# Optimization experiments

Hardware: AMD Instinct MI355X
Metric: run time of the kernel (lower is better)

The kernel has to match this reference:

```python
import jax, jax.numpy as jnp
import numpy as np

N = 50000      # nodes
E = 800000     # edges (avg degree 16)
B = 8          # graphs in batch
H = 128        # hidden (message_passer out_channels)
FF = 64        # fourier_feat_dim -> fourier features have dim 2*FF
REPEATS = 4    # repeats_training
OUT = 4        # output_dim
IN_X = 5
IN_MASK = 3

def _fourier(x, M):
    # https://arxiv.org/pdf/2106.02795.pdf : [cos(xM), sin(xM)] / sqrt(2F)
    p = x @ M
    return jnp.concatenate([jnp.cos(p), jnp.sin(p)], axis=-1) / jnp.sqrt(2.0 * M.shape[1])

def _seg_mean(v, idx, n):
    s = jax.ops.segment_sum(v, idx, num_segments=n)
    c = jax.ops.segment_sum(jnp.ones((v.shape[0],), v.dtype), idx, num_segments=n)
    return s / jnp.maximum(c, 1.0)[:, None]

def setup_inputs() -> dict:
    key = jax.random.key(0)
    ks = jax.random.split(key, 16)
    x = jax.random.normal(ks[0], (N, IN_X), jnp.float32)
    x_mask = jax.random.bernoulli(ks[1], 0.1, (N, IN_MASK)).astype(jnp.float32)
    edge_index = jax.random.randint(ks[2], (2, E), 0, N)
    edge_attr = jax.random.normal(ks[3], (E, 3), jnp.float32)
    pos = jax.random.uniform(ks[4], (N, 2), jnp.float32)
    batch = jnp.sort(jax.random.randint(ks[5], (N,), 0, B))
    sampling_points = jax.random.uniform(ks[6], (2,), jnp.float32)
    fourier_mat = jax.random.normal(ks[7], (2, FF), jnp.float32)  # learnable, init N(0,1)
    W_enc = jax.random.normal(ks[8], (IN_X + IN_MASK, H), jnp.float32) * 0.1
    b_enc = jnp.zeros((H,), jnp.float32)
    W_msg = jax.random.normal(ks[9], (2 * H + 3, H), jnp.float32) * 0.05
    b_msg = jnp.zeros((H,), jnp.float32)
    W_upd = jax.random.normal(ks[10], (4 * H, H), jnp.float32) * 0.05
    b_upd = jnp.zeros((H,), jnp.float32)
    W_dec = jax.random.normal(ks[11], (H, OUT), jnp.float32) * 0.1
    b_dec = jnp.zeros((OUT,), jnp.float32)
    return dict(x=x, x_mask=x_mask, edge_index=edge_index, edge_attr=edge_attr,
                pos=pos, batch=batch, sampling_points=sampling_points,
                fourier_mat=fourier_mat, W_enc=W_enc, b_enc=b_enc,
                W_msg=W_msg, b_msg=b_msg, W_upd=W_upd, b_upd=b_upd,
                W_dec=W_dec, b_dec=b_dec)

def reference(x, x_mask, edge_index, edge_attr, pos, batch, sampling_points,
              fourier_mat, W_enc, b_enc, W_msg, b_msg, W_upd, b_upd, W_dec, b_dec):
    bc = x_mask[:, -1]                                   # 0/1 BC flag
    x_full = jnp.concatenate([x, x_mask], axis=1)        # x = concat([x, x_mask])
    keys_ff = _fourier(pos, fourier_mat)                 # input fourier features [N, 2F]
    h = jax.nn.relu(x_full @ W_enc + b_enc)              # encoder -> [N, H]

    # x_BC: scatter-mean over BC nodes per graph (computed once)
    bc_sum = jax.ops.segment_sum(h * bc[:, None], batch, num_segments=B)
    bc_cnt = jax.ops.segment_sum(bc, batch, num_segments=B)
    x_BC = bc_sum / jnp.maximum(bc_cnt, 1.0)[:, None]    # [B, H]

    x_graph = _seg_mean(h, batch, B)                     # global_mean_pool [B, H]
    src, dst = edge_index[0], edge_index[1]
    deg = jnp.maximum(jax.ops.segment_sum(jnp.ones((E,), h.dtype), dst, num_segments=N), 1.0)

    for _ in range(REPEATS):  # repeated message passing
        m = jax.nn.relu(jnp.concatenate([h[src], h[dst], edge_attr], axis=1) @ W_msg + b_msg)
        agg = jax.ops.segment_sum(m, dst, num_segments=N) / deg[:, None]  # scatter-mean
        upd_in = jnp.concatenate([h, agg, x_graph[batch], x_BC[batch]], axis=1)
        h = h + jax.nn.relu(upd_in @ W_upd + b_upd)
        x_graph = _seg_mean(h, batch, B)                 # re-pool each repeat

    decoded = h @ W_dec + b_dec                          # [N, OUT]

    # kernelized fourier-feature interpolation at the sampling point
    q = _fourier(sampling_points, fourier_mat)           # [2F]
    nq = q / jnp.linalg.norm(q)
    nk = keys_ff / jnp.linalg.norm(keys_ff, axis=1, keepdims=True)
    vals_sum = h.sum(axis=0)                             # [H]
    kwv = nk.T @ h                                       # [2F, H]
    ks_sum = nk.sum(axis=0)                              # [2F]
    enc = (vals_sum + nq @ kwv) / (N + nq @ ks_sum)      # [H]
    U_sampled = enc @ W_dec + b_dec                      # [OUT]
    # pack (U_sampled, decoded) into one array: row 0 = sampled point, rows 1: = nodes
    return jnp.concatenate([U_sampled[None, :], decoded], axis=0)
```

## Files before the change

### kernel.cpp

```cpp
#include <hip/hip_runtime.h>
#include <math.h>

#define Nn 50000
#define Ee 800000
#define Bb 8
#define ROUNDS 4
#define KWVB 512
#define SCB 196
#define AP 40
#define HP 132
#define KS 40
#define NBK 196
#define P1B 391
#define CHUNK 2047

typedef __attribute__((ext_vector_type(8))) short bf16x8;
typedef __attribute__((ext_vector_type(4))) float f32x4;

__device__ inline short f2bf(float f) {
  union { float f; unsigned u; } v; v.f = f;
  unsigned r = v.u + 0x7fff + ((v.u >> 16) & 1);
  return (short)(r >> 16);
}
__device__ inline float bf2f(short s) {
  union { float f; unsigned u; } v; v.u = ((unsigned)(unsigned short)s) << 16;
  return v.f;
}

__global__ __launch_bounds__(256) void encode_seg(
    const float* __restrict__ x, const float* __restrict__ xm,
    const int* __restrict__ batch, const float* __restrict__ W,
    const float* __restrict__ b, float* __restrict__ h,
    float* __restrict__ gsum, float* __restrict__ gcnt,
    float* __restrict__ bcsum, float* __restrict__ bccnt) {
  __shared__ float xs5[128 * 5];
  __shared__ float xm3[128 * 3];
  __shared__ float ls[Bb * 128];
  __shared__ float lb[Bb * 128];
  __shared__ float lc[Bb], lbc[Bb];
  const int t = threadIdx.x;
  const int nBase = blockIdx.x * 128;
  const int j = t & 127, half = t >> 7;
  const int base5 = nBase * 5, base3 = nBase * 3;
  for (int q = t; q < 640; q += 256) xs5[q] = (base5 + q < Nn * 5) ? x[base5 + q] : 0.f;
  for (int q = t; q < 384; q += 256) xm3[q] = (base3 + q < Nn * 3) ? xm[base3 + q] : 0.f;
  for (int q = t; q < Bb * 128; q += 256) { ls[q] = 0.f; lb[q] = 0.f; }
  if (t < Bb) { lc[t] = 0.f; lbc[t] = 0.f; }
  float Wcol[8];
#pragma unroll
  for (int k = 0; k < 8; k++) Wcol[k] = W[k * 128 + j];
  const float bj = b[j];
  __syncthreads();
  int curb = -1;
  float runh = 0.f, runb = 0.f, runc = 0.f, runbc = 0.f;
  for (int kk = 0; kk < 64; kk++) {
    int i = nBase + kk * 2 + half;
    if (i >= Nn) break;
    int li = i - nBase;
    float acc = bj;
#pragma unroll
    for (int k = 0; k < 5; k++) acc = fmaf(xs5[li * 5 + k], Wcol[k], acc);
#pragma unroll
    for (int k = 0; k < 3; k++) acc = fmaf(xm3[li * 3 + k], Wcol[5 + k], acc);
    float v = fmaxf(acc, 0.f);
    h[(size_t)i * 128 + j] = v;
    float bc = xm3[li * 3 + 2];
    int g = batch[i];
    if (g != curb) {
      if (curb >= 0) {
        atomicAdd(&ls[curb * 128 + j], runh);
        atomicAdd(&lb[curb * 128 + j], runb);
        if (j == 0) { atomicAdd(&lc[curb], runc); atomicAdd(&lbc[curb], runbc); }
      }
      curb = g; runh = runb = runc = runbc = 0.f;
    }
    runh += v; runb += v * bc;
    if (j == 0) { runc += 1.f; runbc += bc; }
  }
  if (curb >= 0) {
    atomicAdd(&ls[curb * 128 + j], runh);
    atomicAdd(&lb[curb * 128 + j], runb);
    if (j == 0) { atomicAdd(&lc[curb], runc); atomicAdd(&lbc[curb], runbc); }
  }
  __syncthreads();
  for (int q = t; q < Bb * 128; q += 256) {
    float a = ls[q], c = lb[q];
    if (a != 0.f) atomicAdd(&gsum[q], a);
    if (c != 0.f) atomicAdd(&bcsum[q], c);
  }
  if (t < Bb) { atomicAdd(&gcnt[t], lc[t]); atomicAdd(&bccnt[t], lbc[t]); }
}

__global__ __launch_bounds__(256) void split_w_kernel(
    const float* __restrict__ Wm, const float* __restrict__ Wu,
    short* __restrict__ Wmt_h, short* __restrict__ Wmt_l,
    short* __restrict__ Wut_h, short* __restrict__ Wut_l) {
  int idx = blockIdx.x * 256 + threadIdx.x;
  if (idx < 32768) {
    int k = idx & 127, n = (idx >> 7) & 127, y = idx >> 14;
    float w = Wm[(size_t)(y * 128 + k) * 128 + n];
    short hi = f2bf(w);
    Wmt_h[idx] = hi;
    Wmt_l[idx] = f2bf(w - bf2f(hi));
  } else if (idx < 65536) {
    int j = idx - 32768;
    int k = j & 255, n = j >> 8;
    float w = Wu[(size_t)k * 128 + n];
    short hi = f2bf(w);
    Wut_h[j] = hi;
    Wut_l[j] = f2bf(w - bf2f(hi));
  }
}

__global__ __launch_bounds__(256) void bkt_cnt(const int* __restrict__ ei,
                                               int* __restrict__ bktcnt) {
  __shared__ int hist[NBK];
  int t = threadIdx.x;
  for (int q = t; q < NBK; q += 256) hist[q] = 0;
  __syncthreads();
  int base = blockIdx.x * CHUNK;
  int end = base + CHUNK < Ee ? base + CHUNK : Ee;
  for (int e = base + t; e < end; e += 256) atomicAdd(&hist[ei[Ee + e] >> 8], 1);
  __syncthreads();
  for (int q = t; q < NBK; q += 256)
    if (hist[q]) atomicAdd(&bktcnt[q], hist[q]);
}
__global__ __launch_bounds__(256) void bkt_scan(const int* __restrict__ bktcnt,
                                                int* __restrict__ bktbase,
                                                int* __restrict__ bktcur) {
  __shared__ int s[256];
  int t = threadIdx.x;
  int v = (t < NBK) ? bktcnt[t] : 0;
  s[t] = v;
  __syncthreads();
  for (int off = 1; off < 256; off <<= 1) {
    int x = (t >= off) ? s[t - off] : 0;
    __syncthreads();
    s[t] += x;
    __syncthreads();
  }
  int ex = s[t] - v;
  if (t < NBK) { bktbase[t] = ex; bktcur[t] = ex; }
  if (t == NBK - 1) bktbase[NBK] = ex + v;
}
__global__ __launch_bounds__(256) void bkt_part(
    const int* __restrict__ ei, const float* __restrict__ ea,
    int* __restrict__ bktcur, int2* __restrict__ recA,
    unsigned char* __restrict__ dlo) {
  __shared__ int hist[NBK], lbase[NBK], lcur[NBK];
  int t = threadIdx.x;
  for (int q = t; q < NBK; q += 256) hist[q] = 0;
  __syncthreads();
  int base = blockIdx.x * CHUNK;
  int end = base + CHUNK < Ee ? base + CHUNK : Ee;
  for (int e = base + t; e < end; e += 256) atomicAdd(&hist[ei[Ee + e] >> 8], 1);
  __syncthreads();
  for (int q = t; q < NBK; q += 256) {
    int c = hist[q];
    lbase[q] = c ? atomicAdd(&bktcur[q], c) : 0;
    lcur[q] = 0;
  }
  __syncthreads();
  for (int e = base + t; e < end; e += 256) {
    int d = ei[Ee + e];
    int bk = d >> 8;
    int p = lbase[bk] + atomicAdd(&lcur[bk], 1);
    unsigned r0 = (unsigned)ei[e] |
                  ((unsigned)(unsigned short)f2bf(ea[3 * (size_t)e + 0]) << 16);
    unsigned r1 = (unsigned)(unsigned short)f2bf(ea[3 * (size_t)e + 1]) |
                  ((unsigned)(unsigned short)f2bf(ea[3 * (size_t)e + 2]) << 16);
    recA[p] = make_int2((int)r0, (int)r1);
    dlo[p] = (unsigned char)(d & 255);
  }
}
__global__ __launch_bounds__(256) void dst_cnt(const int* __restrict__ bktbase,
                                               const unsigned char* __restrict__ dlo,
                                               int* __restrict__ cnt) {
  __shared__ int hh[256];
  int t = threadIdx.x;
  hh[t] = 0;
  __syncthreads();
  int b = blockIdx.x;
  int lo = bktbase[b], hi = bktbase[b + 1];
  for (int i = lo + t; i < hi; i += 256) atomicAdd(&hh[dlo[i]], 1);
  __syncthreads();
  int d = b * 256 + t;
  if (d < Nn) cnt[d] = hh[t];
}
__global__ __launch_bounds__(256) void bsum_kernel(const int* __restrict__ cnt,
                                                   int* __restrict__ bsum) {
  __shared__ int wsum[4];
  int t = threadIdx.x;
  int i = blockIdx.x * 256 + t;
  int v = (i < Nn) ? cnt[i] : 0;
#pragma unroll
  for (int off = 32; off > 0; off >>= 1) v += __shfl_down(v, off);
  if ((t & 63) == 0) wsum[t >> 6] = v;
  __syncthreads();
  if (t == 0) bsum[blockIdx.x] = wsum[0] + wsum[1] + wsum[2] + wsum[3];
}
__global__ __launch_bounds__(256) void scan_top_kernel(const int* __restrict__ bsum,
                                                       int* __restrict__ boff) {
  __shared__ int s[256];
  int t = threadIdx.x;
  int v = (t < SCB) ? bsum[t] : 0;
  s[t] = v;
  __syncthreads();
  for (int off = 1; off < 256; off <<= 1) {
    int x = (t >= off) ? s[t - off] : 0;
    __syncthreads();
    s[t] += x;
    __syncthreads();
  }
  boff[t] = s[t] - v;
}
__global__ __launch_bounds__(256) void apply_kernel(
    const int* __restrict__ cnt, const int* __restrict__ boff,
    int* __restrict__ rowptr, float* __restrict__ invdeg) {
  __shared__ int s[256];
  int t = threadIdx.x;
  int i = blockIdx.x * 256 + t;
  int v = (i < Nn) ? cnt[i] : 0;
  s[t] = v;
  __syncthreads();
  for (int off = 1; off < 256; off <<= 1) {
    int x = (t >= off) ? s[t - off] : 0;
    __syncthreads();
    s[t] += x;
    __syncthreads();
  }
  int ex = boff[blockIdx.x] + s[t] - v;
  if (i < Nn) {
    rowptr[i] = ex;
    invdeg[i] = 1.0f / fmaxf((float)v, 1.0f);
    if (i == Nn - 1) rowptr[Nn] = ex + v;
  }
}
__global__ __launch_bounds__(256) void bkt_fin(
    const int* __restrict__ bktbase, const int2* __restrict__ recA,
    const unsigned char* __restrict__ dlo, const int* __restrict__ rowptr,
    int2* __restrict__ rec) {
  __shared__ int cur[256];
  int t = threadIdx.x;
  int b = blockIdx.x;
  int d = b * 256 + t;
  cur[t] = (d < Nn) ? rowptr[d] : 0;
  __syncthreads();
  int lo = bktbase[b], hi = bktbase[b + 1];
  for (int i = lo + t; i < hi; i += 256) {
    int dl = dlo[i];
    int p = atomicAdd(&cur[dl], 1);
    rec[p] = recA[i];
  }
}

__global__ __launch_bounds__(128) void gb_static_kernel(
    const float* __restrict__ bcsum, const float* __restrict__ bccnt,
    const float* __restrict__ Wu, const float* __restrict__ bu,
    float* __restrict__ gbst) {
  __shared__ float xb[128];
  int g = blockIdx.x, t = threadIdx.x;
  xb[t] = bcsum[g * 128 + t] / fmaxf(bccnt[g], 1.f);
  __syncthreads();
  float acc = bu[t];
#pragma unroll 4
  for (int k = 0; k < 128; k++) acc = fmaf(xb[k], Wu[(size_t)(384 + k) * 128 + t], acc);
  gbst[g * 128 + t] = acc;
}

__global__ __launch_bounds__(128) void gb_dyn_kernel(
    const float* __restrict__ gsum, const float* __restrict__ gcnt,
    const float* __restrict__ gbst, const float* __restrict__ Wu,
    float* __restrict__ gb) {
  __shared__ float xg[128];
  int g = blockIdx.x, t = threadIdx.x;
  xg[t] = gsum[g * 128 + t] / fmaxf(gcnt[g], 1.f);
  __syncthreads();
  float acc = gbst[g * 128 + t];
#pragma unroll 4
  for (int k = 0; k < 128; k++) acc = fmaf(xg[k], Wu[(size_t)(256 + k) * 128 + t], acc);
  gb[g * 128 + t] = acc;
}

__global__ __launch_bounds__(256) void proj_mfma(
    const float* __restrict__ h, const short* __restrict__ Wth,
    unsigned char* __restrict__ hs8, unsigned short* __restrict__ hdbf) {
  __shared__ short Ah_s[128 * AP];
  __shared__ short Bh_s[128 * AP];
  const int t = threadIdx.x;
  const int nBase = blockIdx.x * 128;
  const int yoff = blockIdx.y * 16384;
  const int wave = t >> 6, lane = t & 63;
  const int ml = lane & 15, quad = lane >> 4;
  const int ko = quad * 8;

  f32x4 acc[2][8];
#pragma unroll
  for (int nt = 0; nt < 2; nt++)
#pragma unroll
    for (int mt = 0; mt < 8; mt++)
#pragma unroll
      for (int q = 0; q < 4; q++) acc[nt][mt][q] = 0.f;

  const int srow = t >> 1;
  const int kc = (t & 1) * 16;
  const int nd0 = nBase + srow;
  const int nn = nd0 < Nn ? nd0 : Nn - 1;

  for (int c = 0; c < 4; c++) {
    const float* p = &h[(size_t)nn * 128 + c * 32 + kc];
    float4 u0 = *(const float4*)(p + 0);
    float4 u1 = *(const float4*)(p + 4);
    float4 u2 = *(const float4*)(p + 8);
    float4 u3 = *(const float4*)(p + 12);
    const int k0 = c * 32;
    const bf16x8 gb0 = *(const bf16x8*)&Wth[(size_t)yoff + srow * 128 + k0 + kc];
    const bf16x8 gb1 = *(const bf16x8*)&Wth[(size_t)yoff + srow * 128 + k0 + kc + 8];
    float xs[16] = {u0.x,u0.y,u0.z,u0.w, u1.x,u1.y,u1.z,u1.w,
                    u2.x,u2.y,u2.z,u2.w, u3.x,u3.y,u3.z,u3.w};
    bf16x8 vh0, vh1;
#pragma unroll
    for (int j = 0; j < 8; j++) vh0[j] = f2bf(xs[j]);
#pragma unroll
    for (int j = 0; j < 8; j++) vh1[j] = f2bf(xs[8 + j]);
    __syncthreads();
    *(bf16x8*)&Ah_s[srow * AP + kc] = vh0;
    *(bf16x8*)&Ah_s[srow * AP + kc + 8] = vh1;
    *(bf16x8*)&Bh_s[srow * AP + kc] = gb0;
    *(bf16x8*)&Bh_s[srow * AP + kc + 8] = gb1;
    __syncthreads();
#pragma unroll
    for (int mt = 0; mt < 8; mt++) {
      const int ar = (mt * 16 + ml) * AP + ko;
      bf16x8 ah = *(const bf16x8*)&Ah_s[ar];
#pragma unroll
      for (int nt = 0; nt < 2; nt++) {
        const int br = (wave * 32 + nt * 16 + ml) * AP + ko;
        bf16x8 bh = *(const bf16x8*)&Bh_s[br];
        acc[nt][mt] = __builtin_amdgcn_mfma_f32_16x16x32_bf16(ah, bh, acc[nt][mt], 0, 0, 0);
      }
    }
  }
  if (blockIdx.y == 0) {
#pragma unroll
    for (int nt = 0; nt < 2; nt++) {
      const int ch = wave * 32 + nt * 16 + ml;
#pragma unroll
      for (int mt = 0; mt < 8; mt++) {
#pragma unroll
        for (int q = 0; q < 4; q++) {
          int nd = nBase + mt * 16 + quad * 4 + q;
          if (nd < Nn) {
            int pk = __builtin_amdgcn_cvt_pk_fp8_f32(acc[nt][mt][q], acc[nt][mt][q], 0, false);
            hs8[(size_t)nd * 128 + ch] = (unsigned char)(pk & 0xff);
          }
        }
      }
    }
  } else {
#pragma unroll
    for (int nt = 0; nt < 2; nt++) {
      const int ch = wave * 32 + nt * 16 + ml;
#pragma unroll
      for (int mt = 0; mt < 8; mt++) {
#pragma unroll
        for (int q = 0; q < 4; q++) {
          int nd = nBase + mt * 16 + quad * 4 + q;
          if (nd < Nn) hdbf[(size_t)nd * 128 + ch] = (unsigned short)f2bf(acc[nt][mt][q]);
        }
      }
    }
  }
}

__global__ __launch_bounds__(256) void agg_kernel(
    const unsigned char* __restrict__ hs8, const unsigned short* __restrict__ hdbf,
    unsigned short* __restrict__ aggbf, const int2* __restrict__ rec,
    const int* __restrict__ rowptr, const float* __restrict__ invdeg,
    const float* __restrict__ Wm, const float* __restrict__ bm) {
  int t = threadIdx.x;
  int hw = t >> 5, lane = t & 31;
  int v = blockIdx.x * 8 + hw;
  if (v >= Nn) return;
  int c0 = lane * 4;
  const float4 We0 = *(const float4*)&Wm[(size_t)256 * 128 + c0];
  const float4 We1 = *(const float4*)&Wm[(size_t)257 * 128 + c0];
  const float4 We2 = *(const float4*)&Wm[(size_t)258 * 128 + c0];
  const float4 b4  = *(const float4*)&bm[c0];
  const ushort4 hd4 = *(const ushort4*)&hdbf[(size_t)v * 128 + c0];
  const float bx = b4.x + bf2f((short)hd4.x), by = b4.y + bf2f((short)hd4.y),
              bz = b4.z + bf2f((short)hd4.z), bw = b4.w + bf2f((short)hd4.w);
  float ax = 0.f, ay = 0.f, az = 0.f, aw = 0.f;
  float ax2 = 0.f, ay2 = 0.f, az2 = 0.f, aw2 = 0.f;
  const int r0 = rowptr[v], r1 = rowptr[v + 1];
  int e = r0;
  for (; e + 2 <= r1; e += 2) {
    int2 q0 = rec[e], q1 = rec[e + 1];
    int s0 = q0.x & 0xffff, s1 = q1.x & 0xffff;
    unsigned hr0 = *(const unsigned*)&hs8[(size_t)s0 * 128 + c0];
    unsigned hr1 = *(const unsigned*)&hs8[(size_t)s1 * 128 + c0];
    float e00 = bf2f((short)(q0.x >> 16));
    float e01 = bf2f((short)(q0.y & 0xffff));
    float e02 = bf2f((short)(q0.y >> 16));
    float e10 = bf2f((short)(q1.x >> 16));
    float e11 = bf2f((short)(q1.y & 0xffff));
    float e12 = bf2f((short)(q1.y >> 16));
    float h0x = __builtin_amdgcn_cvt_f32_fp8(hr0, 0);
    float h0y = __builtin_amdgcn_cvt_f32_fp8(hr0, 1);
    float h0z = __builtin_amdgcn_cvt_f32_fp8(hr0, 2);
    float h0w = __builtin_amdgcn_cvt_f32_fp8(hr0, 3);
    float h1x = __builtin_amdgcn_cvt_f32_fp8(hr1, 0);
    float h1y = __builtin_amdgcn_cvt_f32_fp8(hr1, 1);
    float h1z = __builtin_amdgcn_cvt_f32_fp8(hr1, 2);
    float h1w = __builtin_amdgcn_cvt_f32_fp8(hr1, 3);
    ax += fmaxf(fmaf(e00, We0.x, fmaf(e01, We1.x, fmaf(e02, We2.x, h0x + bx))), 0.f);
    ay += fmaxf(fmaf(e00, We0.y, fmaf(e01, We1.y, fmaf(e02, We2.y, h0y + by))), 0.f);
    az += fmaxf(fmaf(e00, We0.z, fmaf(e01, We1.z, fmaf(e02, We2.z, h0z + bz))), 0.f);
    aw += fmaxf(fmaf(e00, We0.w, fmaf(e01, We1.w, fmaf(e02, We2.w, h0w + bw))), 0.f);
    ax2 += fmaxf(fmaf(e10, We0.x, fmaf(e11, We1.x, fmaf(e12, We2.x, h1x + bx))), 0.f);
    ay2 += fmaxf(fmaf(e10, We0.y, fmaf(e11, We1.y, fmaf(e12, We2.y, h1y + by))), 0.f);
    az2 += fmaxf(fmaf(e10, We0.z, fmaf(e11, We1.z, fmaf(e12, We2.z, h1z + bz))), 0.f);
    aw2 += fmaxf(fmaf(e10, We0.w, fmaf(e11, We1.w, fmaf(e12, We2.w, h1w + bw))), 0.f);
  }
  if (e < r1) {
    int2 q0 = rec[e];
    int s0 = q0.x & 0xffff;
    unsigned hr0 = *(const unsigned*)&hs8[(size_t)s0 * 128 + c0];
    float e00 = bf2f((short)(q0.x >> 16));
    float e01 = bf2f((short)(q0.y & 0xffff));
    float e02 = bf2f((short)(q0.y >> 16));
    float h0x = __builtin_amdgcn_cvt_f32_fp8(hr0, 0);
    float h0y = __builtin_amdgcn_cvt_f32_fp8(hr0, 1);
    float h0z = __builtin_amdgcn_cvt_f32_fp8(hr0, 2);
    float h0w = __builtin_amdgcn_cvt_f32_fp8(hr0, 3);
    ax += fmaxf(fmaf(e00, We0.x, fmaf(e01, We1.x, fmaf(e02, We2.x, h0x + bx))), 0.f);
    ay += fmaxf(fmaf(e00, We0.y, fmaf(e01, We1.y, fmaf(e02, We2.y, h0y + by))), 0.f);
    az += fmaxf(fmaf(e00, We0.z, fmaf(e01, We1.z, fmaf(e02, We2.z, h0z + bz))), 0.f);
    aw += fmaxf(fmaf(e00, We0.w, fmaf(e01, We1.w, fmaf(e02, We2.w, h0w + bw))), 0.f);
  }
  const float idg = invdeg[v];
  ushort4 o;
  o.x = (unsigned short)f2bf((ax + ax2) * idg);
  o.y = (unsigned short)f2bf((ay + ay2) * idg);
  o.z = (unsigned short)f2bf((az + az2) * idg);
  o.w = (unsigned short)f2bf((aw + aw2) * idg);
  *(ushort4*)&aggbf[(size_t)v * 128 + c0] = o;
}

__global__ __launch_bounds__(256) void updg_mfma(
    float* __restrict__ h, const unsigned short* __restrict__ aggbf,
    const int* __restrict__ batch,
    const short* __restrict__ Wth, const short* __restrict__ Wtl,
    const float* __restrict__ gb, float* __restrict__ gsum_out) {
  __shared__ short Ah_s[128 * AP], Al_s[128 * AP];
  __shared__ short Bh_s[128 * AP], Bl_s[128 * AP];
  __shared__ float gbs[Bb * 128];
  __shared__ float ls[Bb * 128];
  const int t = threadIdx.x;
  const int nBase = blockIdx.x * 128;
  *(float4*)&gbs[t * 4] = *(const float4*)&gb[t * 4];
#pragma unroll
  for (int q = 0; q < 4; q++) ls[t + q * 256] = 0.f;

  const int wave = t >> 6, lane = t & 63;
  const int ml = lane & 15, quad = lane >> 4;
  const int ko = quad * 8;

  f32x4 acc[2][8];
#pragma unroll
  for (int nt = 0; nt < 2; nt++)
#pragma unroll
    for (int mt = 0; mt < 8; mt++)
#pragma unroll
      for (int q = 0; q < 4; q++) acc[nt][mt][q] = 0.f;

  const int srow = t >> 1;
  const int kc = (t & 1) * 16;
  const int nd0 = nBase + srow;
  const int nn = nd0 < Nn ? nd0 : Nn - 1;

  for (int c = 0; c < 8; c++) {
    const int k0 = c * 32;
    bf16x8 vh0, vh1, vl0, vl1;
    if (c < 4) {
      const float* p = &h[(size_t)nn * 128 + c * 32 + kc];
      float4 u0 = *(const float4*)(p + 0);
      float4 u1 = *(const float4*)(p + 4);
      float4 u2 = *(const float4*)(p + 8);
      float4 u3 = *(const float4*)(p + 12);
      float xs[16] = {u0.x,u0.y,u0.z,u0.w, u1.x,u1.y,u1.z,u1.w,
                      u2.x,u2.y,u2.z,u2.w, u3.x,u3.y,u3.z,u3.w};
#pragma unroll
      for (int j = 0; j < 8; j++) {
        short hi = f2bf(xs[j]);
        vh0[j] = hi; vl0[j] = f2bf(xs[j] - bf2f(hi));
      }
#pragma unroll
      for (int j = 0; j < 8; j++) {
        short hi = f2bf(xs[8 + j]);
        vh1[j] = hi; vl1[j] = f2bf(xs[8 + j] - bf2f(hi));
      }
    } else {
      const unsigned short* pa = &aggbf[(size_t)nn * 128 + (c - 4) * 32 + kc];
      vh0 = *(const bf16x8*)(pa);
      vh1 = *(const bf16x8*)(pa + 8);
    }
    const bf16x8 gb0 = *(const bf16x8*)&Wth[(size_t)srow * 256 + k0 + kc];
    const bf16x8 gb1 = *(const bf16x8*)&Wth[(size_t)srow * 256 + k0 + kc + 8];
    const bf16x8 gl0 = *(const bf16x8*)&Wtl[(size_t)srow * 256 + k0 + kc];
    const bf16x8 gl1 = *(const bf16x8*)&Wtl[(size_t)srow * 256 + k0 + kc + 8];
    __syncthreads();
    *(bf16x8*)&Ah_s[srow * AP + kc] = vh0;
    *(bf16x8*)&Ah_s[srow * AP + kc + 8] = vh1;
    if (c < 4) {
      *(bf16x8*)&Al_s[srow * AP + kc] = vl0;
      *(bf16x8*)&Al_s[srow * AP + kc + 8] = vl1;
    }
    *(bf16x8*)&Bh_s[srow * AP + kc] = gb0;
    *(bf16x8*)&Bh_s[srow * AP + kc + 8] = gb1;
    *(bf16x8*)&Bl_s[srow * AP + kc] = gl0;
    *(bf16x8*)&Bl_s[srow * AP + kc + 8] = gl1;
    __syncthreads();
    if (c < 4) {
#pragma unroll
      for (int mt = 0; mt < 8; mt++) {
        const int ar = (mt * 16 + ml) * AP + ko;
        bf16x8 ah = *(const bf16x8*)&Ah_s[ar];
        bf16x8 al = *(const bf16x8*)&Al_s[ar];
#pragma unroll
        for (int nt = 0; nt < 2; nt++) {
          const int br = (wave * 32 + nt * 16 + ml) * AP + ko;
          bf16x8 bh = *(const bf16x8*)&Bh_s[br];
          bf16x8 bl = *(const bf16x8*)&Bl_s[br];
          acc[nt][mt] = __builtin_amdgcn_mfma_f32_16x16x32_bf16(ah, bh, acc[nt][mt], 0, 0, 0);
          acc[nt][mt] = __builtin_amdgcn_mfma_f32_16x16x32_bf16(ah, bl, acc[nt][mt], 0, 0, 0);
          acc[nt][mt] = __builtin_amdgcn_mfma_f32_16x16x32_bf16(al, bh, acc[nt][mt], 0, 0, 0);
        }
      }
    } else {
#pragma unroll
      for (int mt = 0; mt < 8; mt++) {
        const int ar = (mt * 16 + ml) * AP + ko;
        bf16x8 ah = *(const bf16x8*)&Ah_s[ar];
#pragma unroll
        for (int nt = 0; nt < 2; nt++) {
          const int br = (wave * 32 + nt * 16 + ml) * AP + ko;
          bf16x8 bh = *(const bf16x8*)&Bh_s[br];
          bf16x8 bl = *(const bf16x8*)&Bl_s[br];
          acc[nt][mt] = __builtin_amdgcn_mfma_f32_16x16x32_bf16(ah, bh, acc[nt][mt], 0, 0, 0);
          acc[nt][mt] = __builtin_amdgcn_mfma_f32_16x16x32_bf16(ah, bl, acc[nt][mt], 0, 0, 0);
        }
      }
    }
  }
#pragma unroll
  for (int nt = 0; nt < 2; nt++) {
    const int ch = wave * 32 + nt * 16 + ml;
#pragma unroll
    for (int mt = 0; mt < 8; mt++) {
      int rbase = nBase + mt * 16 + quad * 4;
      float runv = 0.f;
      int curb = -1;
#pragma unroll
      for (int q = 0; q < 4; q++) {
        int nd = rbase + q;
        if (nd < Nn) {
          int bi = batch[nd];
          float u = fmaxf(acc[nt][mt][q] + gbs[bi * 128 + ch], 0.f);
          float hn = h[(size_t)nd * 128 + ch] + u;
          h[(size_t)nd * 128 + ch] = hn;
          if (bi != curb) {
            if (curb >= 0) atomicAdd(&ls[curb * 128 + ch], runv);
            curb = bi;
            runv = 0.f;
          }
          runv += hn;
        }
      }
      if (curb >= 0) atomicAdd(&ls[curb * 128 + ch], runv);
    }
  }
  __syncthreads();
#pragma unroll
  for (int q = 0; q < 4; q++) {
    int idx = t + q * 256;
    float v = ls[idx];
    if (v != 0.f) atomicAdd(&gsum_out[idx], v);
  }
}

__global__ __launch_bounds__(256) void kwv_kernel(
    const float* __restrict__ h, const float* __restrict__ pos,
    const float* __restrict__ Fm, const float* __restrict__ Wd,
    const float* __restrict__ bd, float* __restrict__ partial,
    float* __restrict__ ksum, float* __restrict__ out) {
  __shared__ float h_s[32 * HP];
  __shared__ short nkT[128 * KS];
  __shared__ short hT[128 * KS];
  __shared__ float wd[512];
  __shared__ float ksum_s[128];
  __shared__ float dsum[256];
  const int t = threadIdx.x;
  const int hr = t >> 3;
  const int hc = (t & 7) * 16;
  const int fg = (t & 7) * 8;
  const int wave = t >> 6, lane = t & 63;
  const int ml = lane & 15, quad = lane >> 4;
  const int ko = quad * 8;
  if (t < 128) { *(float4*)&wd[t * 4] = *(const float4*)&Wd[t * 4]; ksum_s[t] = 0.f; }
  const float bdv = bd[t & 3];
  const int dn = (t & 127) >> 2, dno = t & 3;
  const int dk0 = (t >> 7) * 64;
  f32x4 acc[2][8];
#pragma unroll
  for (int nt = 0; nt < 2; nt++)
#pragma unroll
    for (int mt = 0; mt < 8; mt++)
#pragma unroll
      for (int q = 0; q < 4; q++) acc[nt][mt][q] = 0.f;
  float klc[8], kls[8];
#pragma unroll
  for (int f = 0; f < 8; f++) { klc[f] = 0.f; kls[f] = 0.f; }

  int ptile = -1;
  const int nTiles = (Nn + 31) / 32;
  for (int tile = blockIdx.x; tile < nTiles; tile += gridDim.x) {
    const int gh = tile * 32 + hr;
    float4 hv0 = {0.f, 0.f, 0.f, 0.f}, hv1 = hv0, hv2 = hv0, hv3 = hv0;
    float cbuf[8], sbuf[8];
    if (gh < Nn) {
      const float* hp = &h[(size_t)gh * 128 + hc];
      hv0 = *(const float4*)(hp + 0);
      hv1 = *(const float4*)(hp + 4);
      hv2 = *(const float4*)(hp + 8);
      hv3 = *(const float4*)(hp + 12);
      const float px = pos[gh * 2 + 0], py = pos[gh * 2 + 1];
#pragma unroll
      for (int f = 0; f < 8; f++) {
        float p = px * Fm[fg + f] + py * Fm[64 + fg + f];
        cbuf[f] = cosf(p) * 0.125f;
        sbuf[f] = sinf(p) * 0.125f;
      }
    } else {
#pragma unroll
      for (int f = 0; f < 8; f++) { cbuf[f] = 0.f; sbuf[f] = 0.f; }
    }
    float xs[16] = {hv0.x,hv0.y,hv0.z,hv0.w, hv1.x,hv1.y,hv1.z,hv1.w,
                    hv2.x,hv2.y,hv2.z,hv2.w, hv3.x,hv3.y,hv3.z,hv3.w};
    __syncthreads();
    if (ptile >= 0 && t < 128) {
      int gn = ptile * 32 + dn;
      if (gn < Nn) out[4 + (size_t)gn * 4 + dno] = dsum[t] + dsum[t + 128] + bdv;
    }
    *(float4*)&h_s[hr * HP + hc + 0]  = hv0;
    *(float4*)&h_s[hr * HP + hc + 4]  = hv1;
    *(float4*)&h_s[hr * HP + hc + 8]  = hv2;
    *(float4*)&h_s[hr * HP + hc + 12] = hv3;
#pragma unroll
    for (int i = 0; i < 16; i++) hT[(hc + i) * KS + hr] = f2bf(xs[i]);
#pragma unroll
    for (int f = 0; f < 8; f++) {
      nkT[(fg + f) * KS + hr] = f2bf(cbuf[f]);
      nkT[(64 + fg + f) * KS + hr] = f2bf(sbuf[f]);
      klc[f] += cbuf[f];
      kls[f] += sbuf[f];
    }
    __syncthreads();
#pragma unroll
    for (int mt = 0; mt < 8; mt++) {
      bf16x8 ah = *(const bf16x8*)&nkT[(mt * 16 + ml) * KS + ko];
#pragma unroll
      for (int nt = 0; nt < 2; nt++) {
        bf16x8 bh = *(const bf16x8*)&hT[(wave * 32 + nt * 16 + ml) * KS + ko];
        acc[nt][mt] = __builtin_amdgcn_mfma_f32_16x16x32_bf16(ah, bh, acc[nt][mt], 0, 0, 0);
      }
    }
    {
      float s = 0.f;
#pragma unroll 4
      for (int kk = dk0; kk < dk0 + 64; kk++) {
        int k = (kk + dn) & 127;
        s = fmaf(h_s[dn * HP + k], wd[k * 4 + dno], s);
      }
      dsum[t] = s;
    }
    ptile = tile;
  }
  __syncthreads();
  if (ptile >= 0 && t < 128) {
    int gn = ptile * 32 + dn;
    if (gn < Nn) out[4 + (size_t)gn * 4 + dno] = dsum[t] + dsum[t + 128] + bdv;
  }
  float* pb = &partial[(size_t)blockIdx.x * 16384];
#pragma unroll
  for (int nt = 0; nt < 2; nt++) {
    const int col = wave * 32 + nt * 16 + ml;
#pragma unroll
    for (int mt = 0; mt < 8; mt++) {
#pragma unroll
      for (int q = 0; q < 4; q++) {
        int row = mt * 16 + quad * 4 + q;
        pb[row * 128 + col] = acc[nt][mt][q];
      }
    }
  }
#pragma unroll
  for (int f = 0; f < 8; f++) {
    atomicAdd(&ksum_s[fg + f], klc[f]);
    atomicAdd(&ksum_s[64 + fg + f], kls[f]);
  }
  __syncthreads();
  if (t < 128) atomicAdd(&ksum[t], ksum_s[t]);
}

__global__ __launch_bounds__(256) void kwv_reduce(const float* __restrict__ partial,
                                                  float* __restrict__ kwv) {
  int idx = blockIdx.x * 256 + threadIdx.x;
  float s = 0.f;
  for (int b = 0; b < KWVB; b++) s += partial[(size_t)b * 16384 + idx];
  kwv[idx] = s;
}

__global__ __launch_bounds__(128) void final_kernel(
    const float* __restrict__ sp, const float* __restrict__ Fm,
    const float* __restrict__ kwv, const float* __restrict__ vs,
    const float* __restrict__ ksum, const float* __restrict__ Wd,
    const float* __restrict__ bd, float* __restrict__ out) {
  __shared__ float nq_s[128];
  __shared__ float red[2];
  __shared__ float redU[8];
  int t = threadIdx.x;
  int jj = t & 63;
  float p = sp[0] * Fm[jj] + sp[1] * Fm[64 + jj];
  nq_s[t] = ((t < 64) ? cosf(p) : sinf(p)) * 0.125f;
  __syncthreads();
  float num = 0.f;
#pragma unroll
  for (int g = 0; g < Bb; g++) num += vs[g * 128 + t];
  for (int k = 0; k < 128; k++) num = fmaf(nq_s[k], kwv[k * 128 + t], num);
  float dp = nq_s[t] * ksum[t];
#pragma unroll
  for (int off = 32; off > 0; off >>= 1) dp += __shfl_down(dp, off);
  if ((t & 63) == 0) red[t >> 6] = dp;
  __syncthreads();
  float den = (float)Nn + red[0] + red[1];
  float e = num / den;
  float u[4];
#pragma unroll
  for (int o = 0; o < 4; o++) u[o] = e * Wd[t * 4 + o];
#pragma unroll
  for (int off = 32; off > 0; off >>= 1) {
#pragma unroll
    for (int o = 0; o < 4; o++) u[o] += __shfl_down(u[o], off);
  }
  if ((t & 63) == 0) {
#pragma unroll
    for (int o = 0; o < 4; o++) redU[(t >> 6) * 4 + o] = u[o];
  }
  __syncthreads();
  if (t < 4) out[t] = redU[t] + redU[4 + t] + bd[t];
}

extern "C" void kernel_launch(void* const* d_in, const int* in_sizes, int n_in,
                              void* d_out, int out_size, void* d_ws, size_t ws_size,
                              hipStream_t stream) {
  const float* x    = (const float*)d_in[0];
  const float* xm   = (const float*)d_in[1];
  const int*   ei   = (const int*)d_in[2];
  const float* ea   = (const float*)d_in[3];
  const float* pos  = (const float*)d_in[4];
  const int*   batch= (const int*)d_in[5];
  const float* sp   = (const float*)d_in[6];
  const float* Fm   = (const float*)d_in[7];
  const float* Wenc = (const float*)d_in[8];
  const float* benc = (const float*)d_in[9];
  const float* Wmsg = (const float*)d_in[10];
  const float* bmsg = (const float*)d_in[11];
  const float* Wupd = (const float*)d_in[12];
  const float* bupd = (const float*)d_in[13];
  const float* Wdec = (const float*)d_in[14];
  const float* bdec = (const float*)d_in[15];
  float* out = (float*)d_out;

  float* ws     = (float*)d_ws;
  float* h      = ws;
  float* agg    = h + (size_t)Nn * 128;
  float* aux    = agg + (size_t)Nn * 128;
  float* invdeg = aux + (size_t)Nn * 128;
  float* gsum   = invdeg + Nn;
  float* gcnt   = gsum + 1024;
  float* bcsum  = gcnt + 8;
  float* bccnt  = bcsum + 1024;
  float* gsumR  = bccnt + 8;
  float* vsum   = gsumR + 4096;
  float* ksum   = vsum + 128;
  float* gbst   = ksum + 128;
  float* gbuf   = gbst + 1024;
  float* kwv    = gbuf + 4096;
  int2*  rec    = (int2*)(kwv + 16384);
  int*   cnt    = (int*)(rec + Ee);
  int*   rowptr = cnt + Nn;
  int*   bsum   = rowptr + Nn + 1;
  int*   boff   = bsum + 256;
  int*   bktcnt = boff + 256;
  int*   bktbase= bktcnt + 196;
  int*   bktcur = bktbase + 197;
  short* wmt_h  = (short*)(bktcur + 196);
  short* wmt_l  = wmt_h + 32768;
  short* wut_h  = wmt_l + 32768;
  short* wut_l  = wut_h + 32768;
  int2*  recA   = (int2*)(wut_l + 32768);
  unsigned char* dlo = (unsigned char*)(recA + Ee);

  unsigned short* aggbf = (unsigned short*)agg;
  unsigned char*  hs8   = (unsigned char*)aux;
  unsigned short* hdbf  = (unsigned short*)(hs8 + (size_t)Nn * 128);

  hipMemsetAsync(gsum, 0, 6416 * sizeof(float), stream);
  hipMemsetAsync(bktcnt, 0, 196 * sizeof(int), stream);

  split_w_kernel<<<256, 256, 0, stream>>>(Wmsg, Wupd, wmt_h, wmt_l, wut_h, wut_l);

  bkt_cnt<<<P1B, 256, 0, stream>>>(ei, bktcnt);
  bkt_scan<<<1, 256, 0, stream>>>(bktcnt, bktbase, bktcur);
  bkt_part<<<P1B, 256, 0, stream>>>(ei, ea, bktcur, recA, dlo);
  dst_cnt<<<NBK, 256, 0, stream>>>(bktbase, dlo, cnt);
  bsum_kernel<<<SCB, 256, 0, stream>>>(cnt, bsum);
  scan_top_kernel<<<1, 256, 0, stream>>>(bsum, boff);
  apply_kernel<<<SCB, 256, 0, stream>>>(cnt, boff, rowptr, invdeg);
  bkt_fin<<<NBK, 256, 0, stream>>>(bktbase, recA, dlo, rowptr, rec);

  const int nb128 = (Nn + 127) / 128;
  encode_seg<<<nb128, 256, 0, stream>>>(x, xm, batch, Wenc, benc, h,
                                        gsum, gcnt, bcsum, bccnt);
  gb_static_kernel<<<Bb, 128, 0, stream>>>(bcsum, bccnt, Wupd, bupd, gbst);
  gb_dyn_kernel<<<Bb, 128, 0, stream>>>(gsum, gcnt, gbst, Wupd, gbuf);

  for (int r = 0; r < ROUNDS; r++) {
    proj_mfma<<<dim3(nb128, 2), 256, 0, stream>>>(h, wmt_h, hs8, hdbf);
    agg_kernel<<<(Nn + 7) / 8, 256, 0, stream>>>(hs8, hdbf, aggbf, rec, rowptr,
                                                 invdeg, Wmsg, bmsg);
    updg_mfma<<<nb128, 256, 0, stream>>>(h, aggbf, batch, wut_h, wut_l,
                                         gbuf + r * 1024, gsumR + r * 1024);
    if (r < ROUNDS - 1)
      gb_dyn_kernel<<<Bb, 128, 0, stream>>>(gsumR + r * 1024, gcnt, gbst, Wupd,
                                            gbuf + (r + 1) * 1024);
  }

  kwv_kernel<<<KWVB, 256, 0, stream>>>(h, pos, Fm, Wdec, bdec, agg, ksum, out);
  kwv_reduce<<<64, 256, 0, stream>>>(agg, kwv);
  final_kernel<<<1, 128, 0, stream>>>(sp, Fm, kwv, gsumR + 3 * 1024, ksum,
                                      Wdec, bdec, out);
}
```

Baseline: 675.5 us.

## Halve MFMA node tile to 64 rows and fuse CSR-build kernels

The projection and update MFMA kernels now process 64 nodes per block instead of 128. This halves the accumulator registers and A-tile shared memory, doubles the grid size for better occupancy across CUs, and re-maps the A-tile loading to four threads per row. Separately, the per-destination count kernel now also emits block sums, and the rowptr apply step is fused with the bucket finalize scatter, removing two launches and a rowptr reload. The trade-off is that each block loads the weight tile once per 64 rows, so weight traffic from L2 doubles.

```diff
diff --git a/kernel.cpp b/kernel.cpp
--- a/kernel.cpp
+++ b/kernel.cpp
@@ -173,10 +173,11 @@
     dlo[p] = (unsigned char)(d & 255);
   }
 }
-__global__ __launch_bounds__(256) void dst_cnt(const int* __restrict__ bktbase,
-                                               const unsigned char* __restrict__ dlo,
-                                               int* __restrict__ cnt) {
+__global__ __launch_bounds__(256) void dst_cnt_bsum(
+    const int* __restrict__ bktbase, const unsigned char* __restrict__ dlo,
+    int* __restrict__ cnt, int* __restrict__ bsum) {
   __shared__ int hh[256];
+  __shared__ int wsum[4];
   int t = threadIdx.x;
   hh[t] = 0;
   __syncthreads();
@@ -185,19 +186,13 @@
   for (int i = lo + t; i < hi; i += 256) atomicAdd(&hh[dlo[i]], 1);
   __syncthreads();
   int d = b * 256 + t;
-  if (d < Nn) cnt[d] = hh[t];
-}
-__global__ __launch_bounds__(256) void bsum_kernel(const int* __restrict__ cnt,
-                                                   int* __restrict__ bsum) {
-  __shared__ int wsum[4];
-  int t = threadIdx.x;
-  int i = blockIdx.x * 256 + t;
-  int v = (i < Nn) ? cnt[i] : 0;
+  int v = hh[t];
+  if (d < Nn) cnt[d] = v;
 #pragma unroll
   for (int off = 32; off > 0; off >>= 1) v += __shfl_down(v, off);
   if ((t & 63) == 0) wsum[t >> 6] = v;
   __syncthreads();
-  if (t == 0) bsum[blockIdx.x] = wsum[0] + wsum[1] + wsum[2] + wsum[3];
+  if (t == 0) bsum[b] = wsum[0] + wsum[1] + wsum[2] + wsum[3];
 }
 __global__ __launch_bounds__(256) void scan_top_kernel(const int* __restrict__ bsum,
                                                        int* __restrict__ boff) {
@@ -214,12 +209,16 @@
   }
   boff[t] = s[t] - v;
 }
-__global__ __launch_bounds__(256) void apply_kernel(
+__global__ __launch_bounds__(256) void apply_fin(
     const int* __restrict__ cnt, const int* __restrict__ boff,
-    int* __restrict__ rowptr, float* __restrict__ invdeg) {
+    const int* __restrict__ bktbase, const int2* __restrict__ recA,
+    const unsigned char* __restrict__ dlo,
+    int* __restrict__ rowptr, float* __restrict__ invdeg,
+    int2* __restrict__ rec) {
   __shared__ int s[256];
-  int t = threadIdx.x;
-  int i = blockIdx.x * 256 + t;
+  __shared__ int cur[256];
+  int t = threadIdx.x, b = blockIdx.x;
+  int i = b * 256 + t;
   int v = (i < Nn) ? cnt[i] : 0;
   s[t] = v;
   __syncthreads();
@@ -229,28 +228,19 @@
     s[t] += x;
     __syncthreads();
   }
-  int ex = boff[blockIdx.x] + s[t] - v;
+  int ex = boff[b] + s[t] - v;
   if (i < Nn) {
     rowptr[i] = ex;
     invdeg[i] = 1.0f / fmaxf((float)v, 1.0f);
     if (i == Nn - 1) rowptr[Nn] = ex + v;
   }
-}
-__global__ __launch_bounds__(256) void bkt_fin(
-    const int* __restrict__ bktbase, const int2* __restrict__ recA,
-    const unsigned char* __restrict__ dlo, const int* __restrict__ rowptr,
-    int2* __restrict__ rec) {
-  __shared__ int cur[256];
-  int t = threadIdx.x;
-  int b = blockIdx.x;
-  int d = b * 256 + t;
-  cur[t] = (d < Nn) ? rowptr[d] : 0;
+  cur[t] = ex;
   __syncthreads();
   int lo = bktbase[b], hi = bktbase[b + 1];
-  for (int i = lo + t; i < hi; i += 256) {
-    int dl = dlo[i];
+  for (int ii = lo + t; ii < hi; ii += 256) {
+    int dl = dlo[ii];
     int p = atomicAdd(&cur[dl], 1);
-    rec[p] = recA[i];
+    rec[p] = recA[ii];
   }
 }
 
@@ -285,52 +275,48 @@
 __global__ __launch_bounds__(256) void proj_mfma(
     const float* __restrict__ h, const short* __restrict__ Wth,
     unsigned char* __restrict__ hs8, unsigned short* __restrict__ hdbf) {
-  __shared__ short Ah_s[128 * AP];
+  __shared__ short Ah_s[64 * AP];
   __shared__ short Bh_s[128 * AP];
   const int t = threadIdx.x;
-  const int nBase = blockIdx.x * 128;
+  const int nBase = blockIdx.x * 64;
   const int yoff = blockIdx.y * 16384;
   const int wave = t >> 6, lane = t & 63;
   const int ml = lane & 15, quad = lane >> 4;
   const int ko = quad * 8;
 
-  f32x4 acc[2][8];
+  f32x4 acc[2][4];
 #pragma unroll
   for (int nt = 0; nt < 2; nt++)
 #pragma unroll
-    for (int mt = 0; mt < 8; mt++)
+    for (int mt = 0; mt < 4; mt++)
 #pragma unroll
       for (int q = 0; q < 4; q++) acc[nt][mt][q] = 0.f;
 
-  const int srow = t >> 1;
+  const int arow = t >> 2;
+  const int kq = (t & 3) * 8;
+  const int brow = t >> 1;
   const int kc = (t & 1) * 16;
-  const int nd0 = nBase + srow;
+  const int nd0 = nBase + arow;
   const int nn = nd0 < Nn ? nd0 : Nn - 1;
 
   for (int c = 0; c < 4; c++) {
-    const float* p = &h[(size_t)nn * 128 + c * 32 + kc];
+    const int k0 = c * 32;
+    const float* p = &h[(size_t)nn * 128 + k0 + kq];
     float4 u0 = *(const float4*)(p + 0);
     float4 u1 = *(const float4*)(p + 4);
-    float4 u2 = *(const float4*)(p + 8);
-    float4 u3 = *(const float4*)(p + 12);
-    const int k0 = c * 32;
-    const bf16x8 gb0 = *(const bf16x8*)&Wth[(size_t)yoff + srow * 128 + k0 + kc];
-    const bf16x8 gb1 = *(const bf16x8*)&Wth[(size_t)yoff + srow * 128 + k0 + kc + 8];
-    float xs[16] = {u0.x,u0.y,u0.z,u0.w, u1.x,u1.y,u1.z,u1.w,
-                    u2.x,u2.y,u2.z,u2.w, u3.x,u3.y,u3.z,u3.w};
-    bf16x8 vh0, vh1;
+    const bf16x8 gb0 = *(const bf16x8*)&Wth[(size_t)yoff + brow * 128 + k0 + kc];
+    const bf16x8 gb1 = *(const bf16x8*)&Wth[(size_t)yoff + brow * 128 + k0 + kc + 8];
+    float xs[8] = {u0.x, u0.y, u0.z, u0.w, u1.x, u1.y, u1.z, u1.w};
+    bf16x8 vh0;
 #pragma unroll
     for (int j = 0; j < 8; j++) vh0[j] = f2bf(xs[j]);
-#pragma unroll
-    for (int j = 0; j < 8; j++) vh1[j] = f2bf(xs[8 + j]);
-    __syncthreads();
-    *(bf16x8*)&Ah_s[srow * AP + kc] = vh0;
-    *(bf16x8*)&Ah_s[srow * AP + kc + 8] = vh1;
-    *(bf16x8*)&Bh_s[srow * AP + kc] = gb0;
-    *(bf16x8*)&Bh_s[srow * AP + kc + 8] = gb1;
-    __syncthreads();
-#pragma unroll
-    for (int mt = 0; mt < 8; mt++) {
+    __syncthreads();
+    *(bf16x8*)&Ah_s[arow * AP + kq] = vh0;
+    *(bf16x8*)&Bh_s[brow * AP + kc] = gb0;
+    *(bf16x8*)&Bh_s[brow * AP + kc + 8] = gb1;
+    __syncthreads();
+#pragma unroll
+    for (int mt = 0; mt < 4; mt++) {
       const int ar = (mt * 16 + ml) * AP + ko;
       bf16x8 ah = *(const bf16x8*)&Ah_s[ar];
 #pragma unroll
@@ -346,7 +332,7 @@
     for (int nt = 0; nt < 2; nt++) {
       const int ch = wave * 32 + nt * 16 + ml;
 #pragma unroll
-      for (int mt = 0; mt < 8; mt++) {
+      for (int mt = 0; mt < 4; mt++) {
 #pragma unroll
         for (int q = 0; q < 4; q++) {
           int nd = nBase + mt * 16 + quad * 4 + q;
@@ -362,7 +348,7 @@
     for (int nt = 0; nt < 2; nt++) {
       const int ch = wave * 32 + nt * 16 + ml;
 #pragma unroll
-      for (int mt = 0; mt < 8; mt++) {
+      for (int mt = 0; mt < 4; mt++) {
 #pragma unroll
         for (int q = 0; q < 4; q++) {
           int nd = nBase + mt * 16 + quad * 4 + q;
@@ -452,12 +438,12 @@
     const int* __restrict__ batch,
     const short* __restrict__ Wth, const short* __restrict__ Wtl,
     const float* __restrict__ gb, float* __restrict__ gsum_out) {
-  __shared__ short Ah_s[128 * AP], Al_s[128 * AP];
+  __shared__ short Ah_s[64 * AP], Al_s[64 * AP];
   __shared__ short Bh_s[128 * AP], Bl_s[128 * AP];
   __shared__ float gbs[Bb * 128];
   __shared__ float ls[Bb * 128];
   const int t = threadIdx.x;
-  const int nBase = blockIdx.x * 128;
+  const int nBase = blockIdx.x * 64;
   *(float4*)&gbs[t * 4] = *(const float4*)&gb[t * 4];
 #pragma unroll
   for (int q = 0; q < 4; q++) ls[t + q * 256] = 0.f;
@@ -466,64 +452,52 @@
   const int ml = lane & 15, quad = lane >> 4;
   const int ko = quad * 8;
 
-  f32x4 acc[2][8];
+  f32x4 acc[2][4];
 #pragma unroll
   for (int nt = 0; nt < 2; nt++)
 #pragma unroll
-    for (int mt = 0; mt < 8; mt++)
+    for (int mt = 0; mt < 4; mt++)
 #pragma unroll
       for (int q = 0; q < 4; q++) acc[nt][mt][q] = 0.f;
 
-  const int srow = t >> 1;
+  const int arow = t >> 2;
+  const int kq = (t & 3) * 8;
+  const int brow = t >> 1;
   const int kc = (t & 1) * 16;
-  const int nd0 = nBase + srow;
+  const int nd0 = nBase + arow;
   const int nn = nd0 < Nn ? nd0 : Nn - 1;
 
   for (int c = 0; c < 8; c++) {
     const int k0 = c * 32;
-    bf16x8 vh0, vh1, vl0, vl1;
+    bf16x8 vh0, vl0;
     if (c < 4) {
-      const float* p = &h[(size_t)nn * 128 + c * 32 + kc];
+      const float* p = &h[(size_t)nn * 128 + k0 + kq];
       float4 u0 = *(const float4*)(p + 0);
       float4 u1 = *(const float4*)(p + 4);
-      float4 u2 = *(const float4*)(p + 8);
-      float4 u3 = *(const float4*)(p + 12);
-      float xs[16] = {u0.x,u0.y,u0.z,u0.w, u1.x,u1.y,u1.z,u1.w,
-                      u2.x,u2.y,u2.z,u2.w, u3.x,u3.y,u3.z,u3.w};
+      float xs[8] = {u0.x, u0.y, u0.z, u0.w, u1.x, u1.y, u1.z, u1.w};
 #pragma unroll
       for (int j = 0; j < 8; j++) {
         short hi = f2bf(xs[j]);
         vh0[j] = hi; vl0[j] = f2bf(xs[j] - bf2f(hi));
       }
-#pragma unroll
-      for (int j = 0; j < 8; j++) {
-        short hi = f2bf(xs[8 + j]);
-        vh1[j] = hi; vl1[j] = f2bf(xs[8 + j] - bf2f(hi));
-      }
     } else {
-      const unsigned short* pa = &aggbf[(size_t)nn * 128 + (c - 4) * 32 + kc];
-      vh0 = *(const bf16x8*)(pa);
-      vh1 = *(const bf16x8*)(pa + 8);
-    }
-    const bf16x8 gb0 = *(const bf16x8*)&Wth[(size_t)srow * 256 + k0 + kc];
-    const bf16x8 gb1 = *(const bf16x8*)&Wth[(size_t)srow * 256 + k0 + kc + 8];
-    const bf16x8 gl0 = *(const bf16x8*)&Wtl[(size_t)srow * 256 + k0 + kc];
-    const bf16x8 gl1 = *(const bf16x8*)&Wtl[(size_t)srow * 256 + k0 + kc + 8];
-    __syncthreads();
-    *(bf16x8*)&Ah_s[srow * AP + kc] = vh0;
-    *(bf16x8*)&Ah_s[srow * AP + kc + 8] = vh1;
+      vh0 = *(const bf16x8*)&aggbf[(size_t)nn * 128 + (c - 4) * 32 + kq];
+    }
+    const bf16x8 gb0 = *(const bf16x8*)&Wth[(size_t)brow * 256 + k0 + kc];
+    const bf16x8 gb1 = *(const bf16x8*)&Wth[(size_t)brow * 256 + k0 + kc + 8];
+    const bf16x8 gl0 = *(const bf16x8*)&Wtl[(size_t)brow * 256 + k0 + kc];
+    const bf16x8 gl1 = *(const bf16x8*)&Wtl[(size_t)brow * 256 + k0 + kc + 8];
+    __syncthreads();
+    *(bf16x8*)&Ah_s[arow * AP + kq] = vh0;
+    if (c < 4) *(bf16x8*)&Al_s[arow * AP + kq] = vl0;
+    *(bf16x8*)&Bh_s[brow * AP + kc] = gb0;
+    *(bf16x8*)&Bh_s[brow * AP + kc + 8] = gb1;
+    *(bf16x8*)&Bl_s[brow * AP + kc] = gl0;
+    *(bf16x8*)&Bl_s[brow * AP + kc + 8] = gl1;
+    __syncthreads();
     if (c < 4) {
-      *(bf16x8*)&Al_s[srow * AP + kc] = vl0;
-      *(bf16x8*)&Al_s[srow * AP + kc + 8] = vl1;
-    }
-    *(bf16x8*)&Bh_s[srow * AP + kc] = gb0;
-    *(bf16x8*)&Bh_s[srow * AP + kc + 8] = gb1;
-    *(bf16x8*)&Bl_s[srow * AP + kc] = gl0;
-    *(bf16x8*)&Bl_s[srow * AP + kc + 8] = gl1;
-    __syncthreads();
-    if (c < 4) {
-#pragma unroll
-      for (int mt = 0; mt < 8; mt++) {
+#pragma unroll
+      for (int mt = 0; mt < 4; mt++) {
         const int ar = (mt * 16 + ml) * AP + ko;
         bf16x8 ah = *(const bf16x8*)&Ah_s[ar];
         bf16x8 al = *(const bf16x8*)&Al_s[ar];
@@ -539,7 +513,7 @@
       }
     } else {
 #pragma unroll
-      for (int mt = 0; mt < 8; mt++) {
+      for (int mt = 0; mt < 4; mt++) {
         const int ar = (mt * 16 + ml) * AP + ko;
         bf16x8 ah = *(const bf16x8*)&Ah_s[ar];
 #pragma unroll
@@ -557,7 +531,7 @@
   for (int nt = 0; nt < 2; nt++) {
     const int ch = wave * 32 + nt * 16 + ml;
 #pragma unroll
-    for (int mt = 0; mt < 8; mt++) {
+    for (int mt = 0; mt < 4; mt++) {
       int rbase = nBase + mt * 16 + quad * 4;
       float runv = 0.f;
       int curb = -1;
@@ -824,24 +798,24 @@
   bkt_cnt<<<P1B, 256, 0, stream>>>(ei, bktcnt);
   bkt_scan<<<1, 256, 0, stream>>>(bktcnt, bktbase, bktcur);
   bkt_part<<<P1B, 256, 0, stream>>>(ei, ea, bktcur, recA, dlo);
-  dst_cnt<<<NBK, 256, 0, stream>>>(bktbase, dlo, cnt);
-  bsum_kernel<<<SCB, 256, 0, stream>>>(cnt, bsum);
+  dst_cnt_bsum<<<NBK, 256, 0, stream>>>(bktbase, dlo, cnt, bsum);
   scan_top_kernel<<<1, 256, 0, stream>>>(bsum, boff);
-  apply_kernel<<<SCB, 256, 0, stream>>>(cnt, boff, rowptr, invdeg);
-  bkt_fin<<<NBK, 256, 0, stream>>>(bktbase, recA, dlo, rowptr, rec);
+  apply_fin<<<NBK, 256, 0, stream>>>(cnt, boff, bktbase, recA, dlo,
+                                     rowptr, invdeg, rec);
 
   const int nb128 = (Nn + 127) / 128;
+  const int nb64  = (Nn + 63) / 64;
   encode_seg<<<nb128, 256, 0, stream>>>(x, xm, batch, Wenc, benc, h,
                                         gsum, gcnt, bcsum, bccnt);
   gb_static_kernel<<<Bb, 128, 0, stream>>>(bcsum, bccnt, Wupd, bupd, gbst);
   gb_dyn_kernel<<<Bb, 128, 0, stream>>>(gsum, gcnt, gbst, Wupd, gbuf);
 
   for (int r = 0; r < ROUNDS; r++) {
-    proj_mfma<<<dim3(nb128, 2), 256, 0, stream>>>(h, wmt_h, hs8, hdbf);
+    proj_mfma<<<dim3(nb64, 2), 256, 0, stream>>>(h, wmt_h, hs8, hdbf);
     agg_kernel<<<(Nn + 7) / 8, 256, 0, stream>>>(hs8, hdbf, aggbf, rec, rowptr,
                                                  invdeg, Wmsg, bmsg);
-    updg_mfma<<<nb128, 256, 0, stream>>>(h, aggbf, batch, wut_h, wut_l,
-                                         gbuf + r * 1024, gsumR + r * 1024);
+    updg_mfma<<<nb64, 256, 0, stream>>>(h, aggbf, batch, wut_h, wut_l,
+                                        gbuf + r * 1024, gsumR + r * 1024);
     if (r < ROUNDS - 1)
       gb_dyn_kernel<<<Bb, 128, 0, stream>>>(gsumR + r * 1024, gcnt, gbst, Wupd,
                                             gbuf + (r + 1) * 1024);
```

New measurement: 643.0 us. 1.05x faster.
